# Optimization experiments

Measured on AMD Instinct MI355X. Metric: run time of the kernel, lower is better.

Reference implementation:

```python
import jax, jax.numpy as jnp
import numpy as np

EPS = 1e-6
HEADS = 8

def _ln_cf(x, w, b):
    # ConvNeXt-style channels_first LayerNorm over C axis of (B,C,H,W)
    mu = jnp.mean(x, axis=1, keepdims=True)
    var = jnp.mean((x - mu) ** 2, axis=1, keepdims=True)
    xn = (x - mu) / jnp.sqrt(var + EPS)
    return xn * w[None, :, None, None] + b[None, :, None, None]

def _xattn(q_map, kv_map, Wq, Wk, Wv, Wo, bo):
    B, C, H, W = q_map.shape
    HW = H * W
    dh = C // HEADS
    xq = q_map.reshape(B, C, HW).transpose(0, 2, 1)   # (B,HW,C)
    xkv = kv_map.reshape(B, C, HW).transpose(0, 2, 1)
    q = (xq @ Wq.T).reshape(B, HW, HEADS, dh).transpose(0, 2, 1, 3)
    k = (xkv @ Wk.T).reshape(B, HW, HEADS, dh).transpose(0, 2, 1, 3)
    v = (xkv @ Wv.T).reshape(B, HW, HEADS, dh).transpose(0, 2, 1, 3)
    scale = dh ** -0.5
    logits = jnp.einsum('bhqd,bhkd->bhqk', q, k) * scale
    attn = jax.nn.softmax(logits, axis=-1)
    o = jnp.einsum('bhqk,bhkd->bhqd', attn, v)        # (B,h,HW,dh)
    o = o.transpose(0, 2, 1, 3).reshape(B, HW, C)
    o = o @ Wo.T + bo
    return o.transpose(0, 2, 1).reshape(B, C, H, W)

def _ffn(x, W1, b1, W2, b2):
    # 1x1 convs == channel-wise linear; exact GELU (torch default)
    h = jnp.einsum('bchw,oc->bohw', x, W1) + b1[None, :, None, None]
    h = jax.nn.gelu(h, approximate=False)
    return jnp.einsum('bchw,oc->bohw', h, W2) + b2[None, :, None, None]

def setup_inputs() -> dict:
    key = jax.random.key(0)
    ks = jax.random.split(key, 24)
    B, C, H, W = 8, 512, 32, 32
    hid = 4 * C
    d = {
        'spatial_feat': jax.random.normal(ks[0], (B, C, H, W), jnp.float32),
        'freq_feat': jax.random.normal(ks[1], (B, C, H, W), jnp.float32),
        # spatial enhancer (standard cross-attn)
        's_Wq': jax.random.normal(ks[2], (C, C), jnp.float32) * 0.02,
        's_Wk': jax.random.normal(ks[3], (C, C), jnp.float32) * 0.02,
        's_Wv': jax.random.normal(ks[4], (C, C), jnp.float32) * 0.02,
        's_Wo': jax.random.normal(ks[5], (C, C), jnp.float32) * 0.02,
        's_bo': jnp.zeros((C,), jnp.float32),
        # frequency enhancer
        'f_Wq': jax.random.normal(ks[6], (C, C), jnp.float32) * 0.02,
        'f_Wk': jax.random.normal(ks[7], (C, C), jnp.float32) * 0.02,
        'f_Wv': jax.random.normal(ks[8], (C, C), jnp.float32) * 0.02,
        'f_Wo': jax.random.normal(ks[9], (C, C), jnp.float32) * 0.02,
        'f_bo': jnp.zeros((C,), jnp.float32),
        # norms
        'sn1_w': jnp.ones((C,), jnp.float32), 'sn1_b': jnp.zeros((C,), jnp.float32),
        'sn2_w': jnp.ones((C,), jnp.float32), 'sn2_b': jnp.zeros((C,), jnp.float32),
        'fn1_w': jnp.ones((C,), jnp.float32), 'fn1_b': jnp.zeros((C,), jnp.float32),
        'fn2_w': jnp.ones((C,), jnp.float32), 'fn2_b': jnp.zeros((C,), jnp.float32),
        # ConvFFNs (1x1 convs)
        'sffn_W1': jax.random.normal(ks[10], (hid, C), jnp.float32) * 0.02,
        'sffn_b1': jnp.zeros((hid,), jnp.float32),
        'sffn_W2': jax.random.normal(ks[11], (C, hid), jnp.float32) * 0.02,
        'sffn_b2': jnp.zeros((C,), jnp.float32),
        'fffn_W1': jax.random.normal(ks[12], (hid, C), jnp.float32) * 0.02,
        'fffn_b1': jnp.zeros((hid,), jnp.float32),
        'fffn_W2': jax.random.normal(ks[13], (C, hid), jnp.float32) * 0.02,
        'fffn_b2': jnp.zeros((C,), jnp.float32),
    }
    return d

def reference(spatial_feat, freq_feat,
              s_Wq, s_Wk, s_Wv, s_Wo, s_bo,
              f_Wq, f_Wk, f_Wv, f_Wo, f_bo,
              sn1_w, sn1_b, sn2_w, sn2_b,
              fn1_w, fn1_b, fn2_w, fn2_b,
              sffn_W1, sffn_b1, sffn_W2, sffn_b2,
              fffn_W1, fffn_b1, fffn_W2, fffn_b2):
    enh_s = _xattn(spatial_feat, freq_feat, s_Wq, s_Wk, s_Wv, s_Wo, s_bo)
    enh_f = _xattn(freq_feat, spatial_feat, f_Wq, f_Wk, f_Wv, f_Wo, f_bo)
    s = _ln_cf(spatial_feat + enh_s, sn1_w, sn1_b)
    s = _ln_cf(s + _ffn(s, sffn_W1, sffn_b1, sffn_W2, sffn_b2), sn2_w, sn2_b)
    f = _ln_cf(freq_feat + enh_f, fn1_w, fn1_b)
    f = _ln_cf(f + _ffn(f, fffn_W1, fffn_b1, fffn_W2, fffn_b2), fn2_w, fn2_b)
    return (s, f)
```

## Files before the change

kernel.cpp:

```cpp
#include <hip/hip_runtime.h>
#include <hip/hip_bf16.h>


#define CCH 512
#define HWD 1024

typedef unsigned short u16;
typedef unsigned int u32;
typedef __attribute__((ext_vector_type(8))) __bf16 bf16x8;
typedef __attribute__((ext_vector_type(4))) float f32x4;
typedef __attribute__((ext_vector_type(4))) unsigned short u16x4;
typedef __attribute__((ext_vector_type(8))) unsigned short u16x8;

__device__ __forceinline__ float bf2f(u16 u) { return __uint_as_float(((u32)u) << 16); }
__device__ __forceinline__ u16 f2bf(float f) {
    u32 u = __float_as_uint(f);
    return (u16)((u + 0x7fffu + ((u >> 16) & 1u)) >> 16);
}
__device__ __forceinline__ float ldp(const void* p, int i, bool isbf) {
    return isbf ? bf2f(((const u16*)p)[i]) : ((const float*)p)[i];
}
__device__ __forceinline__ float fast_gelu(float v) {
    return v * __frcp_rn(1.0f + __expf(-1.702f * v));
}

#define GLL16(g, l) __builtin_amdgcn_global_load_lds( \
    (const __attribute__((address_space(1))) u32*)(g), \
    (__attribute__((address_space(3))) u32*)(l), 16, 0, 0)

struct MMJob { const u16* A; const u16* W; const void* bias; void* Y; };
struct PJob  { const u16* A; const u16* W; u16* Y; int ldY; int gm; int gn; };
struct PJobs { PJob j[6]; };
struct AJob  { const u16* QK; const u16* VT; u16* AO; };
struct LNJob { const u16* A; const float* Br; const void* w; const void* b; void* Y; };

__global__ void k_detect(const u16* __restrict__ in, int* __restrict__ flag) {
    if (threadIdx.x == 0 && blockIdx.x == 0) {
        int sane = 0;
        for (int i = 0; i < 1024; i += 2) {
            int e = (in[i] >> 7) & 0xFF;
            if (e >= 0x6D && e <= 0x8D) sane++;
        }
        *flag = (sane >= 256) ? 1 : 0;
    }
}

struct CvtJobs {
    const void* src[12];
    u16* dst[12];
    int chunk0[13];
};
__global__ __launch_bounds__(256) void k_cvt_all(CvtJobs J, const int* __restrict__ flag) {
    bool isbf = (*flag != 0);
    int b = blockIdx.x;
    int j = 0;
    #pragma unroll
    for (int i = 0; i < 12; i++) if (b >= J.chunk0[i + 1]) j = i + 1;
    int idx = (b - J.chunk0[j]) * 1024 + threadIdx.x * 4;
    u16* d = J.dst[j] + idx;
    if (isbf) {
        *(u16x4*)d = *(const u16x4*)((const u16*)J.src[j] + idx);
    } else {
        float4 v = *(const float4*)((const float*)J.src[j] + idx);
        d[0] = f2bf(v.x); d[1] = f2bf(v.y); d[2] = f2bf(v.z); d[3] = f2bf(v.w);
    }
}

__global__ __launch_bounds__(256) void k_transpose2(const void* __restrict__ in0,
                                                    const void* __restrict__ in1,
                                                    u16* __restrict__ o0,
                                                    u16* __restrict__ o1,
                                                    const int* __restrict__ flag) {
    __shared__ float tile[32][33];
    bool isbf = (*flag != 0);
    int z = blockIdx.z;
    const void* in = (z < 8) ? in0 : in1;
    u16* out = (z < 8) ? o0 : o1;
    int b = z & 7;
    int hw0 = blockIdx.x * 32, c0 = blockIdx.y * 32;
    int tx = threadIdx.x, ty = threadIdx.y;
    size_t base = (size_t)b * CCH * HWD;
    if (isbf) {
        const u16* ip = (const u16*)in + base;
        for (int i = ty; i < 32; i += 8)
            tile[i][tx] = bf2f(ip[(size_t)(c0 + i) * HWD + hw0 + tx]);
    } else {
        const float* ip = (const float*)in + base;
        for (int i = ty; i < 32; i += 8)
            tile[i][tx] = ip[(size_t)(c0 + i) * HWD + hw0 + tx];
    }
    __syncthreads();
    u16* op = out + (size_t)b * HWD * CCH;
    for (int i = ty; i < 32; i += 8)
        op[(size_t)(hw0 + i) * CCH + c0 + tx] = f2bf(tile[tx][i]);
}

__device__ __forceinline__ void swz(int pid, int gm, int gn, int& bm, int& bn) {
    int gsz = 8 * gn;
    int gid = pid / gsz;
    int fm = gid * 8;
    int rows = (gm - fm < 8) ? (gm - fm) : 8;
    int pin = pid - gid * gsz;
    bm = fm + pin % rows;
    bn = pin / rows;
}

__global__ __launch_bounds__(256) void k_mm(MMJob j0, MMJob j1,
                                            int K, int ldY, int mode, int gm, int gn,
                                            const int* __restrict__ flag) {
    __shared__ u16 As[128 * 32], Asb[128 * 32];
    __shared__ u16 Bs[128 * 32], Bsb[128 * 32];
    MMJob J = blockIdx.z ? j1 : j0;
    int t = threadIdx.x;
    int w = t >> 6, l = t & 63;
    int bm, bn;
    swz(blockIdx.x, gm, gn, bm, bn);
    int m0 = bm * 128, n0 = bn * 128;
    int wm = (w >> 1) * 64, wn = (w & 1) * 64;

    int r0 = (w * 2 + 0) * 16 + (l >> 2);
    int r1 = (w * 2 + 1) * 16 + (l >> 2);
    int sg0 = (((l & 3) ^ ((r0 >> 1) & 3))) * 8;
    int sg1 = (((l & 3) ^ ((r1 >> 1) & 3))) * 8;
    const u16* ga0 = J.A + (size_t)(m0 + r0) * K + sg0;
    const u16* ga1 = J.A + (size_t)(m0 + r1) * K + sg1;
    const u16* gb0 = J.W + (size_t)(n0 + r0) * K + sg0;
    const u16* gb1 = J.W + (size_t)(n0 + r1) * K + sg1;
    int lo0 = (w * 2 + 0) * 512, lo1 = (w * 2 + 1) * 512;

    int quad = l >> 4, lr = l & 15;
    int aoff[4], boff[4];
    #pragma unroll
    for (int i = 0; i < 4; i++) {
        int ra = wm + i * 16 + lr, rb = wn + i * 16 + lr;
        aoff[i] = ra * 32 + (quad ^ ((ra >> 1) & 3)) * 8;
        boff[i] = rb * 32 + (quad ^ ((rb >> 1) & 3)) * 8;
    }

    f32x4 acc[4][4] = {};

    for (int k0 = 0; k0 < K; k0 += 64) {
        __syncthreads();
        GLL16(ga0 + k0, &As[lo0]);
        GLL16(ga1 + k0, &As[lo1]);
        GLL16(gb0 + k0, &Bs[lo0]);
        GLL16(gb1 + k0, &Bs[lo1]);
        GLL16(ga0 + k0 + 32, &Asb[lo0]);
        GLL16(ga1 + k0 + 32, &Asb[lo1]);
        GLL16(gb0 + k0 + 32, &Bsb[lo0]);
        GLL16(gb1 + k0 + 32, &Bsb[lo1]);
        __syncthreads();
        {
            bf16x8 af[4], bfr[4];
            #pragma unroll
            for (int i = 0; i < 4; i++) af[i] = *(const bf16x8*)&As[aoff[i]];
            #pragma unroll
            for (int j = 0; j < 4; j++) bfr[j] = *(const bf16x8*)&Bs[boff[j]];
            #pragma unroll
            for (int i = 0; i < 4; i++)
                #pragma unroll
                for (int j = 0; j < 4; j++)
                    acc[i][j] = __builtin_amdgcn_mfma_f32_16x16x32_bf16(af[i], bfr[j], acc[i][j], 0, 0, 0);
        }
        {
            bf16x8 af[4], bfr[4];
            #pragma unroll
            for (int i = 0; i < 4; i++) af[i] = *(const bf16x8*)&Asb[aoff[i]];
            #pragma unroll
            for (int j = 0; j < 4; j++) bfr[j] = *(const bf16x8*)&Bsb[boff[j]];
            #pragma unroll
            for (int i = 0; i < 4; i++)
                #pragma unroll
                for (int j = 0; j < 4; j++)
                    acc[i][j] = __builtin_amdgcn_mfma_f32_16x16x32_bf16(af[i], bfr[j], acc[i][j], 0, 0, 0);
        }
    }

    bool isbf = (*flag != 0);
    #pragma unroll
    for (int i = 0; i < 4; i++) {
        int rowb = m0 + wm + i * 16 + quad * 4;
        #pragma unroll
        for (int j = 0; j < 4; j++) {
            int col = n0 + wn + j * 16 + lr;
            float bv = (mode == 1 || mode == 2) ? ldp(J.bias, col, isbf) : 0.f;
            #pragma unroll
            for (int r = 0; r < 4; r++) {
                float v = acc[i][j][r] + bv;
                if (mode == 2) {
                    ((u16*)J.Y)[(size_t)(rowb + r) * ldY + col] = f2bf(fast_gelu(v));
                } else if (mode == 3) {
                    ((u16*)J.Y)[(size_t)(rowb + r) * ldY + col] = f2bf(v);
                } else {
                    ((float*)J.Y)[(size_t)(rowb + r) * ldY + col] = v;
                }
            }
        }
    }
}

__global__ __launch_bounds__(256) void k_mm64(MMJob j0, MMJob j1,
                                              int K, int ldY, int mode, int gm, int gn,
                                              const int* __restrict__ flag) {
    __shared__ u16 As[128 * 32], Asb[128 * 32];
    __shared__ u16 Bs[64 * 32], Bsb[64 * 32];
    MMJob J = blockIdx.z ? j1 : j0;
    int t = threadIdx.x;
    int w = t >> 6, l = t & 63;
    int bm, bn;
    swz(blockIdx.x, gm, gn, bm, bn);
    int m0 = bm * 128, n0 = bn * 64;
    int wm = (w >> 1) * 64, wn = (w & 1) * 32;

    int r0 = (w * 2 + 0) * 16 + (l >> 2);
    int r1 = (w * 2 + 1) * 16 + (l >> 2);
    int rb_ = w * 16 + (l >> 2);
    int sg0 = (((l & 3) ^ ((r0 >> 1) & 3))) * 8;
    int sg1 = (((l & 3) ^ ((r1 >> 1) & 3))) * 8;
    int sgb = (((l & 3) ^ ((rb_ >> 1) & 3))) * 8;
    const u16* ga0 = J.A + (size_t)(m0 + r0) * K + sg0;
    const u16* ga1 = J.A + (size_t)(m0 + r1) * K + sg1;
    const u16* gb  = J.W + (size_t)(n0 + rb_) * K + sgb;
    int lo0 = (w * 2 + 0) * 512, lo1 = (w * 2 + 1) * 512, lob = w * 512;

    int quad = l >> 4, lr = l & 15;
    int aoff[4], boff[2];
    #pragma unroll
    for (int i = 0; i < 4; i++) {
        int ra = wm + i * 16 + lr;
        aoff[i] = ra * 32 + (quad ^ ((ra >> 1) & 3)) * 8;
    }
    #pragma unroll
    for (int j = 0; j < 2; j++) {
        int rb2 = wn + j * 16 + lr;
        boff[j] = rb2 * 32 + (quad ^ ((rb2 >> 1) & 3)) * 8;
    }

    f32x4 acc[4][2] = {};

    for (int k0 = 0; k0 < K; k0 += 64) {
        __syncthreads();
        GLL16(ga0 + k0, &As[lo0]);
        GLL16(ga1 + k0, &As[lo1]);
        GLL16(gb + k0, &Bs[lob]);
        GLL16(ga0 + k0 + 32, &Asb[lo0]);
        GLL16(ga1 + k0 + 32, &Asb[lo1]);
        GLL16(gb + k0 + 32, &Bsb[lob]);
        __syncthreads();
        {
            bf16x8 af[4], bfr[2];
            #pragma unroll
            for (int i = 0; i < 4; i++) af[i] = *(const bf16x8*)&As[aoff[i]];
            #pragma unroll
            for (int j = 0; j < 2; j++) bfr[j] = *(const bf16x8*)&Bs[boff[j]];
            #pragma unroll
            for (int i = 0; i < 4; i++)
                #pragma unroll
                for (int j = 0; j < 2; j++)
                    acc[i][j] = __builtin_amdgcn_mfma_f32_16x16x32_bf16(af[i], bfr[j], acc[i][j], 0, 0, 0);
        }
        {
            bf16x8 af[4], bfr[2];
            #pragma unroll
            for (int i = 0; i < 4; i++) af[i] = *(const bf16x8*)&Asb[aoff[i]];
            #pragma unroll
            for (int j = 0; j < 2; j++) bfr[j] = *(const bf16x8*)&Bsb[boff[j]];
            #pragma unroll
            for (int i = 0; i < 4; i++)
                #pragma unroll
                for (int j = 0; j < 2; j++)
                    acc[i][j] = __builtin_amdgcn_mfma_f32_16x16x32_bf16(af[i], bfr[j], acc[i][j], 0, 0, 0);
        }
    }

    bool isbf = (*flag != 0);
    #pragma unroll
    for (int i = 0; i < 4; i++) {
        int rowb = m0 + wm + i * 16 + quad * 4;
        #pragma unroll
        for (int j = 0; j < 2; j++) {
            int col = n0 + wn + j * 16 + lr;
            float bv = (mode == 1 || mode == 2) ? ldp(J.bias, col, isbf) : 0.f;
            #pragma unroll
            for (int r = 0; r < 4; r++) {
                float v = acc[i][j][r] + bv;
                if (mode == 2) {
                    ((u16*)J.Y)[(size_t)(rowb + r) * ldY + col] = f2bf(fast_gelu(v));
                } else if (mode == 3) {
                    ((u16*)J.Y)[(size_t)(rowb + r) * ldY + col] = f2bf(v);
                } else {
                    ((float*)J.Y)[(size_t)(rowb + r) * ldY + col] = v;
                }
            }
        }
    }
}

__global__ __launch_bounds__(256) void k_proj(PJobs JJ, const int* __restrict__ flag) {
    __shared__ u16 As[128 * 32], Asb[128 * 32];
    __shared__ u16 Bs[64 * 32], Bsb[64 * 32];
    (void)flag;
    PJob J = JJ.j[blockIdx.z];
    const int K = 512;
    int t = threadIdx.x;
    int w = t >> 6, l = t & 63;
    int bm, bn;
    swz(blockIdx.x, J.gm, J.gn, bm, bn);
    int m0 = bm * 128, n0 = bn * 64;
    int wm = (w >> 1) * 64, wn = (w & 1) * 32;

    int r0 = (w * 2 + 0) * 16 + (l >> 2);
    int r1 = (w * 2 + 1) * 16 + (l >> 2);
    int rb_ = w * 16 + (l >> 2);
    int sg0 = (((l & 3) ^ ((r0 >> 1) & 3))) * 8;
    int sg1 = (((l & 3) ^ ((r1 >> 1) & 3))) * 8;
    int sgb = (((l & 3) ^ ((rb_ >> 1) & 3))) * 8;
    const u16* ga0 = J.A + (size_t)(m0 + r0) * K + sg0;
    const u16* ga1 = J.A + (size_t)(m0 + r1) * K + sg1;
    const u16* gb  = J.W + (size_t)(n0 + rb_) * K + sgb;
    int lo0 = (w * 2 + 0) * 512, lo1 = (w * 2 + 1) * 512, lob = w * 512;

    int quad = l >> 4, lr = l & 15;
    int aoff[4], boff[2];
    #pragma unroll
    for (int i = 0; i < 4; i++) {
        int ra = wm + i * 16 + lr;
        aoff[i] = ra * 32 + (quad ^ ((ra >> 1) & 3)) * 8;
    }
    #pragma unroll
    for (int j = 0; j < 2; j++) {
        int rb2 = wn + j * 16 + lr;
        boff[j] = rb2 * 32 + (quad ^ ((rb2 >> 1) & 3)) * 8;
    }

    f32x4 acc[4][2] = {};

    for (int k0 = 0; k0 < K; k0 += 64) {
        __syncthreads();
        GLL16(ga0 + k0, &As[lo0]);
        GLL16(ga1 + k0, &As[lo1]);
        GLL16(gb + k0, &Bs[lob]);
        GLL16(ga0 + k0 + 32, &Asb[lo0]);
        GLL16(ga1 + k0 + 32, &Asb[lo1]);
        GLL16(gb + k0 + 32, &Bsb[lob]);
        __syncthreads();
        {
            bf16x8 af[4], bfr[2];
            #pragma unroll
            for (int i = 0; i < 4; i++) af[i] = *(const bf16x8*)&As[aoff[i]];
            #pragma unroll
            for (int j = 0; j < 2; j++) bfr[j] = *(const bf16x8*)&Bs[boff[j]];
            #pragma unroll
            for (int i = 0; i < 4; i++)
                #pragma unroll
                for (int j = 0; j < 2; j++)
                    acc[i][j] = __builtin_amdgcn_mfma_f32_16x16x32_bf16(af[i], bfr[j], acc[i][j], 0, 0, 0);
        }
        {
            bf16x8 af[4], bfr[2];
            #pragma unroll
            for (int i = 0; i < 4; i++) af[i] = *(const bf16x8*)&Asb[aoff[i]];
            #pragma unroll
            for (int j = 0; j < 2; j++) bfr[j] = *(const bf16x8*)&Bsb[boff[j]];
            #pragma unroll
            for (int i = 0; i < 4; i++)
                #pragma unroll
                for (int j = 0; j < 2; j++)
                    acc[i][j] = __builtin_amdgcn_mfma_f32_16x16x32_bf16(af[i], bfr[j], acc[i][j], 0, 0, 0);
        }
    }

    #pragma unroll
    for (int i = 0; i < 4; i++) {
        int rowb = m0 + wm + i * 16 + quad * 4;
        #pragma unroll
        for (int j = 0; j < 2; j++) {
            int col = n0 + wn + j * 16 + lr;
            #pragma unroll
            for (int r = 0; r < 4; r++)
                J.Y[(size_t)(rowb + r) * J.ldY + col] = f2bf(acc[i][j][r]);
        }
    }
}

__global__ __launch_bounds__(256) void k_attn2(AJob j0, AJob j1) {
    __shared__ __align__(16) u16 Ks[2][64][32];
    __shared__ __align__(16) u16 Vs[2][64][32];
    __shared__ __align__(16) u16 U[10240];

    AJob J = blockIdx.y ? j1 : j0;
    int blk = blockIdx.x;
    int t = threadIdx.x;
    int w = t >> 6, l = t & 63;
    int l15 = l & 15, quad = l >> 4;
    int qt = blk >> 6;
    int bh = blk & 63;
    int h = bh & 7, b = bh >> 3;
    int tok0 = b * 1024;
    int q0 = qt * 128;
    int hc = h * 64;

    #pragma unroll
    for (int kc = 0; kc < 2; kc++)
        #pragma unroll
        for (int g = 0; g < 2; g++) {
            int row = w * 32 + g * 16 + (l >> 2);
            int sl = ((l & 3) ^ ((row >> 1) & 3)) * 8;
            const u16* gp = J.QK + (size_t)(tok0 + q0 + row) * 1024 + hc + kc * 32 + sl;
            GLL16(gp, &U[kc * 4096 + (w * 32 + g * 16) * 32]);
        }
    __syncthreads();

    bf16x8 qf[2][2];
    #pragma unroll
    for (int jq = 0; jq < 2; jq++)
        #pragma unroll
        for (int kc = 0; kc < 2; kc++) {
            int row = w * 32 + jq * 16 + l15;
            qf[jq][kc] = *(const bf16x8*)&U[kc * 4096 + row * 32 + (quad ^ ((row >> 1) & 3)) * 8];
        }

    u16* Pw = &U[w * 2560];

    float l_[2] = {0.f, 0.f};
    f32x4 acco[2][4] = {};

    for (int kt = 0; kt < 16; kt++) {
        __syncthreads();
        {
            int row = w * 16 + (l >> 2);
            int f = (row >> 1) & 3;
            int sl = ((l & 3) ^ f) * 8;
            int key = kt * 64 + row;
            #pragma unroll
            for (int kc = 0; kc < 2; kc++) {
                const u16* kp = J.QK + (size_t)(tok0 + key) * 1024 + 512 + hc + kc * 32 + sl;
                GLL16(kp, &Ks[kc][w * 16][0]);
            }
            #pragma unroll
            for (int kck = 0; kck < 2; kck++) {
                const u16* vp = J.VT + (size_t)(hc + row) * 8192 + tok0 + kt * 64 + kck * 32 + sl;
                GLL16(vp, &Vs[kck][w * 16][0]);
            }
        }
        __syncthreads();

        f32x4 accs[4][2] = {};
        #pragma unroll
        for (int kc = 0; kc < 2; kc++) {
            bf16x8 kf[4];
            #pragma unroll
            for (int i = 0; i < 4; i++) {
                int row = i * 16 + l15;
                kf[i] = *(const bf16x8*)&Ks[kc][row][(quad ^ ((row >> 1) & 3)) * 8];
            }
            #pragma unroll
            for (int i = 0; i < 4; i++)
                #pragma unroll
                for (int jq = 0; jq < 2; jq++)
                    accs[i][jq] = __builtin_amdgcn_mfma_f32_16x16x32_bf16(kf[i], qf[jq][kc], accs[i][jq], 0, 0, 0);
        }

        #pragma unroll
        for (int jq = 0; jq < 2; jq++) {
            float ts = 0.f;
            #pragma unroll
            for (int i = 0; i < 4; i++) {
                u16x4 pk;
                #pragma unroll
                for (int r = 0; r < 4; r++) {
                    float p = __expf(accs[i][jq][r] * 0.125f);
                    ts += p;
                    pk[r] = f2bf(p);
                }
                *(u16x4*)&Pw[(jq * 16 + l15) * 80 + i * 16 + quad * 4] = pk;
            }
            ts += __shfl_xor(ts, 16);
            ts += __shfl_xor(ts, 32);
            l_[jq] += ts;
        }

        #pragma unroll
        for (int kck = 0; kck < 2; kck++) {
            bf16x8 pf[2], vf[4];
            #pragma unroll
            for (int i2 = 0; i2 < 2; i2++)
                pf[i2] = *(const bf16x8*)&Pw[(i2 * 16 + l15) * 80 + kck * 32 + quad * 8];
            #pragma unroll
            for (int jd = 0; jd < 4; jd++) {
                int row = jd * 16 + l15;
                vf[jd] = *(const bf16x8*)&Vs[kck][row][(quad ^ ((row >> 1) & 3)) * 8];
            }
            #pragma unroll
            for (int i2 = 0; i2 < 2; i2++)
                #pragma unroll
                for (int jd = 0; jd < 4; jd++)
                    acco[i2][jd] = __builtin_amdgcn_mfma_f32_16x16x32_bf16(pf[i2], vf[jd], acco[i2][jd], 0, 0, 0);
        }
    }

    #pragma unroll
    for (int i2 = 0; i2 < 2; i2++) {
        float linv = 1.0f / l_[i2];
        #pragma unroll
        for (int r = 0; r < 4; r++) {
            float li = __shfl(linv, quad * 4 + r);
            int token = tok0 + q0 + w * 32 + i2 * 16 + quad * 4 + r;
            u16* dst = J.AO + (size_t)token * 512 + hc;
            #pragma unroll
            for (int jd = 0; jd < 4; jd++)
                dst[jd * 16 + l15] = f2bf(acco[i2][jd][r] * li);
        }
    }
}

__global__ __launch_bounds__(256) void k_ln(LNJob j0, LNJob j1,
                                            const int* __restrict__ flag) {
    LNJob J = blockIdx.y ? j1 : j0;
    bool isbf = (*flag != 0);
    int token = blockIdx.x * 4 + (threadIdx.x >> 6);
    int lane = threadIdx.x & 63;
    int c0 = lane * 8;
    const u16* pa = J.A + (size_t)token * CCH + c0;
    const float* pb = J.Br + (size_t)token * CCH + c0;
    u16x8 av = *(const u16x8*)pa;
    float4 b0 = *(const float4*)pb;
    float4 b1 = *(const float4*)(pb + 4);
    float v[8];
    float s = 0.f, s2 = 0.f;
    #pragma unroll
    for (int u = 0; u < 8; u++) {
        float x = bf2f(av[u]) + ((u < 4) ? (&b0.x)[u] : (&b1.x)[u - 4]);
        v[u] = x; s += x; s2 += x * x;
    }
    #pragma unroll
    for (int off = 32; off > 0; off >>= 1) {
        s += __shfl_xor(s, off);
        s2 += __shfl_xor(s2, off);
    }
    float mu = s * (1.f / CCH);
    float var = s2 * (1.f / CCH) - mu * mu;
    float rstd = rsqrtf(var + 1e-6f);
    u16x8 ov;
    #pragma unroll
    for (int u = 0; u < 8; u++)
        ov[u] = f2bf((v[u] - mu) * rstd * ldp(J.w, c0 + u, isbf) + ldp(J.b, c0 + u, isbf));
    *(u16x8*)((u16*)J.Y + (size_t)token * CCH + c0) = ov;
}

__global__ __launch_bounds__(256) void k_ln_out(LNJob j0, LNJob j1,
                                                void* __restrict__ out, int brBase,
                                                const int* __restrict__ flag) {
    LNJob J = blockIdx.y ? j1 : j0;
    int branch = brBase + blockIdx.y;
    bool isbf = (*flag != 0);
    int token = blockIdx.x * 4 + (threadIdx.x >> 6);
    int lane = threadIdx.x & 63;
    int c0 = lane * 8;
    const u16* pa = J.A + (size_t)token * CCH + c0;
    const float* pb = J.Br + (size_t)token * CCH + c0;
    u16x8 av = *(const u16x8*)pa;
    float4 b0 = *(const float4*)pb;
    float4 b1 = *(const float4*)(pb + 4);
    float v[8];
    float s = 0.f, s2 = 0.f;
    #pragma unroll
    for (int u = 0; u < 8; u++) {
        float x = bf2f(av[u]) + ((u < 4) ? (&b0.x)[u] : (&b1.x)[u - 4]);
        v[u] = x; s += x; s2 += x * x;
    }
    #pragma unroll
    for (int off = 32; off > 0; off >>= 1) {
        s += __shfl_xor(s, off);
        s2 += __shfl_xor(s2, off);
    }
    float mu = s * (1.f / CCH);
    float var = s2 * (1.f / CCH) - mu * mu;
    float rstd = rsqrtf(var + 1e-6f);
    int b = token >> 10, hw = token & 1023;
    size_t obase = (size_t)branch * CCH * HWD * 8 + (size_t)b * CCH * HWD + hw;
    if (isbf) {
        u16* op = (u16*)out + obase;
        #pragma unroll
        for (int u = 0; u < 8; u++) {
            float y = (v[u] - mu) * rstd * ldp(J.w, c0 + u, true) + ldp(J.b, c0 + u, true);
            op[(size_t)(c0 + u) * HWD] = f2bf(y);
        }
    } else {
        float* op = (float*)out + obase;
        #pragma unroll
        for (int u = 0; u < 8; u++) {
            float y = (v[u] - mu) * rstd * ldp(J.w, c0 + u, false) + ldp(J.b, c0 + u, false);
            op[(size_t)(c0 + u) * HWD] = y;
        }
    }
}

extern "C" void kernel_launch(void* const* d_in, const int* in_sizes, int n_in,
                              void* d_out, int out_size, void* d_ws, size_t ws_size,
                              hipStream_t stream) {
    (void)in_sizes; (void)n_in; (void)out_size;

    char* wsb = (char*)d_ws;
    int* flag = (int*)wsb;
    u16* Wall = (u16*)(wsb + 256);
    u16* Xs = (u16*)(wsb + 256 + 12582912);
    u16* Xf = (u16*)(wsb + 256 + 12582912 + 8388608);
    char* rbase = wsb + 29360384;

    const size_t BRSZ = 67108864;
    bool dual = ws_size >= (29360384 + 2 * BRSZ);

    u16* QKb[2]; u16* VTb[2]; u16* AOb[2]; u16* Hbb[2];
    float* ENHb[2];
    for (int b = 0; b < 2; b++) {
        char* r = rbase + (dual ? b * BRSZ : 0);
        QKb[b] = (u16*)r;
        ENHb[b] = (float*)r;
        VTb[b] = (u16*)(r + 16777216);
        AOb[b] = (u16*)(r + 16777216 + 8388608);
        Hbb[b] = (u16*)(r + 16777216 + 2 * 8388608);
    }

    const int SQ = 262144, SW1 = 1048576;
    const u16* Xq[2] = {Xs, Xf};
    const u16* Xkv[2] = {Xf, Xs};
    u16* Wq[2]; u16* Wk[2]; u16* Wv[2]; u16* Wo[2]; u16* W1[2]; u16* W2[2];
    const void *bo[2], *n1w[2], *n1b[2], *n2w[2], *n2b[2], *b1[2], *b2[2];
    for (int b = 0; b < 2; b++) {
        u16* Wb = Wall + (size_t)b * 3145728;
        Wq[b] = Wb; Wk[b] = Wb + SQ; Wv[b] = Wb + 2 * SQ; Wo[b] = Wb + 3 * SQ;
        W1[b] = Wb + 4 * SQ; W2[b] = Wb + 4 * SQ + SW1;
        bo[b]  = d_in[b ? 11 : 6];
        n1w[b] = d_in[b ? 16 : 12]; n1b[b] = d_in[b ? 17 : 13];
        n2w[b] = d_in[b ? 18 : 14]; n2b[b] = d_in[b ? 19 : 15];
        b1[b]  = d_in[b ? 25 : 21]; b2[b]  = d_in[b ? 27 : 23];
    }

    k_detect<<<1, 64, 0, stream>>>((const u16*)d_in[0], flag);

    {
        CvtJobs J;
        int ch = 0;
        for (int b = 0; b < 2; b++) {
            const int srcIdx[6] = {b ? 7 : 2, b ? 8 : 3, b ? 9 : 4, b ? 10 : 5,
                                   b ? 24 : 20, b ? 26 : 22};
            u16* dsts[6] = {Wq[b], Wk[b], Wv[b], Wo[b], W1[b], W2[b]};
            const int sz[6] = {SQ, SQ, SQ, SQ, SW1, SW1};
            for (int i = 0; i < 6; i++) {
                int j = b * 6 + i;
                J.src[j] = d_in[srcIdx[i]];
                J.dst[j] = dsts[i];
                J.chunk0[j] = ch;
                ch += sz[i] / 1024;
            }
        }
        J.chunk0[12] = ch;
        k_cvt_all<<<ch, 256, 0, stream>>>(J, flag);
    }

    dim3 tb(32, 8);
    k_transpose2<<<dim3(32, 16, 16), tb, 0, stream>>>(d_in[0], d_in[1], Xs, Xf, flag);

    auto mmj = [&](const u16* A, const u16* W, const void* bias, void* Y) {
        MMJob j; j.A = A; j.W = W; j.bias = bias; j.Y = Y; return j;
    };
    auto pj = [&](const u16* A, const u16* W, u16* Y, int ldY, int gm, int gn) {
        PJob j; j.A = A; j.W = W; j.Y = Y; j.ldY = ldY; j.gm = gm; j.gn = gn; return j;
    };
    auto lnj = [&](const u16* A, const float* Br, const void* w, const void* bb, void* Y) {
        LNJob j; j.A = A; j.Br = Br; j.w = w; j.b = bb; j.Y = Y; return j;
    };

    int nbr = dual ? 2 : 1;
    int nloop = dual ? 1 : 2;
    for (int it = 0; it < nloop; it++) {
        int b0 = dual ? 0 : it;
        int b1i = dual ? 1 : it;

        {
            PJobs JJ;
            int nz = 0;
            for (int z = 0; z < nbr; z++) {
                int b = dual ? z : it;
                JJ.j[nz++] = pj(Xq[b], Wq[b], QKb[b], 1024, 64, 8);
                JJ.j[nz++] = pj(Xkv[b], Wk[b], QKb[b] + 512, 1024, 64, 8);
                JJ.j[nz++] = pj(Wv[b], Xkv[b], VTb[b], 8192, 4, 128);
            }
            for (int z = nz; z < 6; z++) JJ.j[z] = JJ.j[0];
            k_proj<<<dim3(512, 1, nz), 256, 0, stream>>>(JJ, flag);
        }
        {
            AJob a0, a1;
            a0.QK = QKb[b0]; a0.VT = VTb[b0]; a0.AO = AOb[b0];
            a1.QK = QKb[b1i]; a1.VT = VTb[b1i]; a1.AO = AOb[b1i];
            k_attn2<<<dim3(512, nbr), 256, 0, stream>>>(a0, a1);
        }
        k_mm64<<<dim3(512, 1, nbr), 256, 0, stream>>>(
            mmj(AOb[b0], Wo[b0], bo[b0], ENHb[b0]),
            mmj(AOb[b1i], Wo[b1i], bo[b1i], ENHb[b1i]),
            512, 512, 1, 64, 8, flag);
        k_ln<<<dim3(2048, nbr), 256, 0, stream>>>(
            lnj(Xq[b0], ENHb[b0], n1w[b0], n1b[b0], AOb[b0]),
            lnj(Xq[b1i], ENHb[b1i], n1w[b1i], n1b[b1i], AOb[b1i]), flag);
        k_mm<<<dim3(1024, 1, nbr), 256, 0, stream>>>(
            mmj(AOb[b0], W1[b0], b1[b0], Hbb[b0]),
            mmj(AOb[b1i], W1[b1i], b1[b1i], Hbb[b1i]),
            512, 2048, 2, 64, 16, flag);
        k_mm64<<<dim3(512, 1, nbr), 256, 0, stream>>>(
            mmj(Hbb[b0], W2[b0], b2[b0], ENHb[b0]),
            mmj(Hbb[b1i], W2[b1i], b2[b1i], ENHb[b1i]),
            2048, 512, 1, 64, 8, flag);
        k_ln_out<<<dim3(2048, nbr), 256, 0, stream>>>(
            lnj(AOb[b0], ENHb[b0], n2w[b0], n2b[b0], nullptr),
            lnj(AOb[b1i], ENHb[b1i], n2w[b1i], n2b[b1i], nullptr),
            d_out, dual ? 0 : it, flag);
    }
}
```

Measured before the change: 508.5 us.

## Load GEMM B operand directly into registers and store residual branch in bf16

All three GEMM kernels (k_mm, k_mm64, k_proj) now load the weight (B) operand straight from global memory into registers instead of staging it through LDS with global_load_lds. This halves LDS use and removes LDS reads for B. The Wo and FFN2 GEMM outputs switch to bf16 (new mode 5) and the LayerNorm kernels read them as bf16, which halves that intermediate traffic. The costs are uncoalesced per-lane global loads of W and the extra rounding of the residual branch to bf16.

```diff
diff --git a/kernel.cpp b/kernel.cpp
--- a/kernel.cpp
+++ b/kernel.cpp
@@ -32,7 +32,7 @@
 struct PJob  { const u16* A; const u16* W; u16* Y; int ldY; int gm; int gn; };
 struct PJobs { PJob j[6]; };
 struct AJob  { const u16* QK; const u16* VT; u16* AO; };
-struct LNJob { const u16* A; const float* Br; const void* w; const void* b; void* Y; };
+struct LNJob { const u16* A; const u16* Br; const void* w; const void* b; void* Y; };
 
 __global__ void k_detect(const u16* __restrict__ in, int* __restrict__ flag) {
     if (threadIdx.x == 0 && blockIdx.x == 0) {
@@ -105,11 +105,20 @@
     bn = pin / rows;
 }
 
+__device__ __forceinline__ void ep_store(void* Y, size_t off, float v, int mode) {
+    if (mode == 2) {
+        ((u16*)Y)[off] = f2bf(fast_gelu(v));
+    } else if (mode == 3 || mode == 5) {
+        ((u16*)Y)[off] = f2bf(v);
+    } else {
+        ((float*)Y)[off] = v;
+    }
+}
+
 __global__ __launch_bounds__(256) void k_mm(MMJob j0, MMJob j1,
                                             int K, int ldY, int mode, int gm, int gn,
                                             const int* __restrict__ flag) {
     __shared__ u16 As[128 * 32], Asb[128 * 32];
-    __shared__ u16 Bs[128 * 32], Bsb[128 * 32];
     MMJob J = blockIdx.z ? j1 : j0;
     int t = threadIdx.x;
     int w = t >> 6, l = t & 63;
@@ -124,18 +133,19 @@
     int sg1 = (((l & 3) ^ ((r1 >> 1) & 3))) * 8;
     const u16* ga0 = J.A + (size_t)(m0 + r0) * K + sg0;
     const u16* ga1 = J.A + (size_t)(m0 + r1) * K + sg1;
-    const u16* gb0 = J.W + (size_t)(n0 + r0) * K + sg0;
-    const u16* gb1 = J.W + (size_t)(n0 + r1) * K + sg1;
     int lo0 = (w * 2 + 0) * 512, lo1 = (w * 2 + 1) * 512;
 
     int quad = l >> 4, lr = l & 15;
-    int aoff[4], boff[4];
+    int aoff[4];
     #pragma unroll
     for (int i = 0; i < 4; i++) {
-        int ra = wm + i * 16 + lr, rb = wn + i * 16 + lr;
+        int ra = wm + i * 16 + lr;
         aoff[i] = ra * 32 + (quad ^ ((ra >> 1) & 3)) * 8;
-        boff[i] = rb * 32 + (quad ^ ((rb >> 1) & 3)) * 8;
-    }
+    }
+    const u16* gwb[4];
+    #pragma unroll
+    for (int j = 0; j < 4; j++)
+        gwb[j] = J.W + (size_t)(n0 + wn + j * 16 + lr) * K + quad * 8;
 
     f32x4 acc[4][4] = {};
 
@@ -143,36 +153,34 @@
         __syncthreads();
         GLL16(ga0 + k0, &As[lo0]);
         GLL16(ga1 + k0, &As[lo1]);
-        GLL16(gb0 + k0, &Bs[lo0]);
-        GLL16(gb1 + k0, &Bs[lo1]);
         GLL16(ga0 + k0 + 32, &Asb[lo0]);
         GLL16(ga1 + k0 + 32, &Asb[lo1]);
-        GLL16(gb0 + k0 + 32, &Bsb[lo0]);
-        GLL16(gb1 + k0 + 32, &Bsb[lo1]);
-        __syncthreads();
-        {
-            bf16x8 af[4], bfr[4];
+        bf16x8 b0[4], b1[4];
+        #pragma unroll
+        for (int j = 0; j < 4; j++) {
+            b0[j] = *(const bf16x8*)(gwb[j] + k0);
+            b1[j] = *(const bf16x8*)(gwb[j] + k0 + 32);
+        }
+        __syncthreads();
+        {
+            bf16x8 af[4];
             #pragma unroll
             for (int i = 0; i < 4; i++) af[i] = *(const bf16x8*)&As[aoff[i]];
             #pragma unroll
-            for (int j = 0; j < 4; j++) bfr[j] = *(const bf16x8*)&Bs[boff[j]];
-            #pragma unroll
             for (int i = 0; i < 4; i++)
                 #pragma unroll
                 for (int j = 0; j < 4; j++)
-                    acc[i][j] = __builtin_amdgcn_mfma_f32_16x16x32_bf16(af[i], bfr[j], acc[i][j], 0, 0, 0);
-        }
-        {
-            bf16x8 af[4], bfr[4];
+                    acc[i][j] = __builtin_amdgcn_mfma_f32_16x16x32_bf16(af[i], b0[j], acc[i][j], 0, 0, 0);
+        }
+        {
+            bf16x8 af[4];
             #pragma unroll
             for (int i = 0; i < 4; i++) af[i] = *(const bf16x8*)&Asb[aoff[i]];
             #pragma unroll
-            for (int j = 0; j < 4; j++) bfr[j] = *(const bf16x8*)&Bsb[boff[j]];
-            #pragma unroll
             for (int i = 0; i < 4; i++)
                 #pragma unroll
                 for (int j = 0; j < 4; j++)
-                    acc[i][j] = __builtin_amdgcn_mfma_f32_16x16x32_bf16(af[i], bfr[j], acc[i][j], 0, 0, 0);
+                    acc[i][j] = __builtin_amdgcn_mfma_f32_16x16x32_bf16(af[i], b1[j], acc[i][j], 0, 0, 0);
         }
     }
 
@@ -183,18 +191,10 @@
         #pragma unroll
         for (int j = 0; j < 4; j++) {
             int col = n0 + wn + j * 16 + lr;
-            float bv = (mode == 1 || mode == 2) ? ldp(J.bias, col, isbf) : 0.f;
-            #pragma unroll
-            for (int r = 0; r < 4; r++) {
-                float v = acc[i][j][r] + bv;
-                if (mode == 2) {
-                    ((u16*)J.Y)[(size_t)(rowb + r) * ldY + col] = f2bf(fast_gelu(v));
-                } else if (mode == 3) {
-                    ((u16*)J.Y)[(size_t)(rowb + r) * ldY + col] = f2bf(v);
-                } else {
-                    ((float*)J.Y)[(size_t)(rowb + r) * ldY + col] = v;
-                }
-            }
+            float bv = (mode == 1 || mode == 2 || mode == 5) ? ldp(J.bias, col, isbf) : 0.f;
+            #pragma unroll
+            for (int r = 0; r < 4; r++)
+                ep_store(J.Y, (size_t)(rowb + r) * ldY + col, acc[i][j][r] + bv, mode);
         }
     }
 }
@@ -203,7 +203,6 @@
                                               int K, int ldY, int mode, int gm, int gn,
                                               const int* __restrict__ flag) {
     __shared__ u16 As[128 * 32], Asb[128 * 32];
-    __shared__ u16 Bs[64 * 32], Bsb[64 * 32];
     MMJob J = blockIdx.z ? j1 : j0;
     int t = threadIdx.x;
     int w = t >> 6, l = t & 63;
@@ -214,27 +213,23 @@
 
     int r0 = (w * 2 + 0) * 16 + (l >> 2);
     int r1 = (w * 2 + 1) * 16 + (l >> 2);
-    int rb_ = w * 16 + (l >> 2);
     int sg0 = (((l & 3) ^ ((r0 >> 1) & 3))) * 8;
     int sg1 = (((l & 3) ^ ((r1 >> 1) & 3))) * 8;
-    int sgb = (((l & 3) ^ ((rb_ >> 1) & 3))) * 8;
     const u16* ga0 = J.A + (size_t)(m0 + r0) * K + sg0;
     const u16* ga1 = J.A + (size_t)(m0 + r1) * K + sg1;
-    const u16* gb  = J.W + (size_t)(n0 + rb_) * K + sgb;
-    int lo0 = (w * 2 + 0) * 512, lo1 = (w * 2 + 1) * 512, lob = w * 512;
+    int lo0 = (w * 2 + 0) * 512, lo1 = (w * 2 + 1) * 512;
 
     int quad = l >> 4, lr = l & 15;
-    int aoff[4], boff[2];
+    int aoff[4];
     #pragma unroll
     for (int i = 0; i < 4; i++) {
         int ra = wm + i * 16 + lr;
         aoff[i] = ra * 32 + (quad ^ ((ra >> 1) & 3)) * 8;
     }
-    #pragma unroll
-    for (int j = 0; j < 2; j++) {
-        int rb2 = wn + j * 16 + lr;
-        boff[j] = rb2 * 32 + (quad ^ ((rb2 >> 1) & 3)) * 8;
-    }
+    const u16* gwb[2];
+    #pragma unroll
+    for (int j = 0; j < 2; j++)
+        gwb[j] = J.W + (size_t)(n0 + wn + j * 16 + lr) * K + quad * 8;
 
     f32x4 acc[4][2] = {};
 
@@ -242,34 +237,34 @@
         __syncthreads();
         GLL16(ga0 + k0, &As[lo0]);
         GLL16(ga1 + k0, &As[lo1]);
-        GLL16(gb + k0, &Bs[lob]);
         GLL16(ga0 + k0 + 32, &Asb[lo0]);
         GLL16(ga1 + k0 + 32, &Asb[lo1]);
-        GLL16(gb + k0 + 32, &Bsb[lob]);
-        __syncthreads();
-        {
-            bf16x8 af[4], bfr[2];
+        bf16x8 b0[2], b1[2];
+        #pragma unroll
+        for (int j = 0; j < 2; j++) {
+            b0[j] = *(const bf16x8*)(gwb[j] + k0);
+            b1[j] = *(const bf16x8*)(gwb[j] + k0 + 32);
+        }
+        __syncthreads();
+        {
+            bf16x8 af[4];
             #pragma unroll
             for (int i = 0; i < 4; i++) af[i] = *(const bf16x8*)&As[aoff[i]];
             #pragma unroll
-            for (int j = 0; j < 2; j++) bfr[j] = *(const bf16x8*)&Bs[boff[j]];
-            #pragma unroll
             for (int i = 0; i < 4; i++)
                 #pragma unroll
                 for (int j = 0; j < 2; j++)
-                    acc[i][j] = __builtin_amdgcn_mfma_f32_16x16x32_bf16(af[i], bfr[j], acc[i][j], 0, 0, 0);
-        }
-        {
-            bf16x8 af[4], bfr[2];
+                    acc[i][j] = __builtin_amdgcn_mfma_f32_16x16x32_bf16(af[i], b0[j], acc[i][j], 0, 0, 0);
+        }
+        {
+            bf16x8 af[4];
             #pragma unroll
             for (int i = 0; i < 4; i++) af[i] = *(const bf16x8*)&Asb[aoff[i]];
             #pragma unroll
-            for (int j = 0; j < 2; j++) bfr[j] = *(const bf16x8*)&Bsb[boff[j]];
-            #pragma unroll
             for (int i = 0; i < 4; i++)
                 #pragma unroll
                 for (int j = 0; j < 2; j++)
-                    acc[i][j] = __builtin_amdgcn_mfma_f32_16x16x32_bf16(af[i], bfr[j], acc[i][j], 0, 0, 0);
+                    acc[i][j] = __builtin_amdgcn_mfma_f32_16x16x32_bf16(af[i], b1[j], acc[i][j], 0, 0, 0);
         }
     }
 
@@ -280,25 +275,16 @@
         #pragma unroll
         for (int j = 0; j < 2; j++) {
             int col = n0 + wn + j * 16 + lr;
-            float bv = (mode == 1 || mode == 2) ? ldp(J.bias, col, isbf) : 0.f;
-            #pragma unroll
-            for (int r = 0; r < 4; r++) {
-                float v = acc[i][j][r] + bv;
-                if (mode == 2) {
-                    ((u16*)J.Y)[(size_t)(rowb + r) * ldY + col] = f2bf(fast_gelu(v));
-                } else if (mode == 3) {
-                    ((u16*)J.Y)[(size_t)(rowb + r) * ldY + col] = f2bf(v);
-                } else {
-                    ((float*)J.Y)[(size_t)(rowb + r) * ldY + col] = v;
-                }
-            }
+            float bv = (mode == 1 || mode == 2 || mode == 5) ? ldp(J.bias, col, isbf) : 0.f;
+            #pragma unroll
+            for (int r = 0; r < 4; r++)
+                ep_store(J.Y, (size_t)(rowb + r) * ldY + col, acc[i][j][r] + bv, mode);
         }
     }
 }
 
 __global__ __launch_bounds__(256) void k_proj(PJobs JJ, const int* __restrict__ flag) {
     __shared__ u16 As[128 * 32], Asb[128 * 32];
-    __shared__ u16 Bs[64 * 32], Bsb[64 * 32];
     (void)flag;
     PJob J = JJ.j[blockIdx.z];
     const int K = 512;
@@ -311,27 +297,23 @@
 
     int r0 = (w * 2 + 0) * 16 + (l >> 2);
     int r1 = (w * 2 + 1) * 16 + (l >> 2);
-    int rb_ = w * 16 + (l >> 2);
     int sg0 = (((l & 3) ^ ((r0 >> 1) & 3))) * 8;
     int sg1 = (((l & 3) ^ ((r1 >> 1) & 3))) * 8;
-    int sgb = (((l & 3) ^ ((rb_ >> 1) & 3))) * 8;
     const u16* ga0 = J.A + (size_t)(m0 + r0) * K + sg0;
     const u16* ga1 = J.A + (size_t)(m0 + r1) * K + sg1;
-    const u16* gb  = J.W + (size_t)(n0 + rb_) * K + sgb;
-    int lo0 = (w * 2 + 0) * 512, lo1 = (w * 2 + 1) * 512, lob = w * 512;
+    int lo0 = (w * 2 + 0) * 512, lo1 = (w * 2 + 1) * 512;
 
     int quad = l >> 4, lr = l & 15;
-    int aoff[4], boff[2];
+    int aoff[4];
     #pragma unroll
     for (int i = 0; i < 4; i++) {
         int ra = wm + i * 16 + lr;
         aoff[i] = ra * 32 + (quad ^ ((ra >> 1) & 3)) * 8;
     }
-    #pragma unroll
-    for (int j = 0; j < 2; j++) {
-        int rb2 = wn + j * 16 + lr;
-        boff[j] = rb2 * 32 + (quad ^ ((rb2 >> 1) & 3)) * 8;
-    }
+    const u16* gwb[2];
+    #pragma unroll
+    for (int j = 0; j < 2; j++)
+        gwb[j] = J.W + (size_t)(n0 + wn + j * 16 + lr) * K + quad * 8;
 
     f32x4 acc[4][2] = {};
 
@@ -339,34 +321,34 @@
         __syncthreads();
         GLL16(ga0 + k0, &As[lo0]);
         GLL16(ga1 + k0, &As[lo1]);
-        GLL16(gb + k0, &Bs[lob]);
         GLL16(ga0 + k0 + 32, &Asb[lo0]);
         GLL16(ga1 + k0 + 32, &Asb[lo1]);
-        GLL16(gb + k0 + 32, &Bsb[lob]);
-        __syncthreads();
-        {
-            bf16x8 af[4], bfr[2];
+        bf16x8 b0[2], b1[2];
+        #pragma unroll
+        for (int j = 0; j < 2; j++) {
+            b0[j] = *(const bf16x8*)(gwb[j] + k0);
+            b1[j] = *(const bf16x8*)(gwb[j] + k0 + 32);
+        }
+        __syncthreads();
+        {
+            bf16x8 af[4];
             #pragma unroll
             for (int i = 0; i < 4; i++) af[i] = *(const bf16x8*)&As[aoff[i]];
             #pragma unroll
-            for (int j = 0; j < 2; j++) bfr[j] = *(const bf16x8*)&Bs[boff[j]];
-            #pragma unroll
             for (int i = 0; i < 4; i++)
                 #pragma unroll
                 for (int j = 0; j < 2; j++)
-                    acc[i][j] = __builtin_amdgcn_mfma_f32_16x16x32_bf16(af[i], bfr[j], acc[i][j], 0, 0, 0);
-        }
-        {
-            bf16x8 af[4], bfr[2];
+                    acc[i][j] = __builtin_amdgcn_mfma_f32_16x16x32_bf16(af[i], b0[j], acc[i][j], 0, 0, 0);
+        }
+        {
+            bf16x8 af[4];
             #pragma unroll
             for (int i = 0; i < 4; i++) af[i] = *(const bf16x8*)&Asb[aoff[i]];
             #pragma unroll
-            for (int j = 0; j < 2; j++) bfr[j] = *(const bf16x8*)&Bsb[boff[j]];
-            #pragma unroll
             for (int i = 0; i < 4; i++)
                 #pragma unroll
                 for (int j = 0; j < 2; j++)
-                    acc[i][j] = __builtin_amdgcn_mfma_f32_16x16x32_bf16(af[i], bfr[j], acc[i][j], 0, 0, 0);
+                    acc[i][j] = __builtin_amdgcn_mfma_f32_16x16x32_bf16(af[i], b1[j], acc[i][j], 0, 0, 0);
         }
     }
 
@@ -521,16 +503,13 @@
     int token = blockIdx.x * 4 + (threadIdx.x >> 6);
     int lane = threadIdx.x & 63;
     int c0 = lane * 8;
-    const u16* pa = J.A + (size_t)token * CCH + c0;
-    const float* pb = J.Br + (size_t)token * CCH + c0;
-    u16x8 av = *(const u16x8*)pa;
-    float4 b0 = *(const float4*)pb;
-    float4 b1 = *(const float4*)(pb + 4);
+    u16x8 av = *(const u16x8*)(J.A + (size_t)token * CCH + c0);
+    u16x8 bv = *(const u16x8*)(J.Br + (size_t)token * CCH + c0);
     float v[8];
     float s = 0.f, s2 = 0.f;
     #pragma unroll
     for (int u = 0; u < 8; u++) {
-        float x = bf2f(av[u]) + ((u < 4) ? (&b0.x)[u] : (&b1.x)[u - 4]);
+        float x = bf2f(av[u]) + bf2f(bv[u]);
         v[u] = x; s += x; s2 += x * x;
     }
     #pragma unroll
@@ -557,16 +536,13 @@
     int token = blockIdx.x * 4 + (threadIdx.x >> 6);
     int lane = threadIdx.x & 63;
     int c0 = lane * 8;
-    const u16* pa = J.A + (size_t)token * CCH + c0;
-    const float* pb = J.Br + (size_t)token * CCH + c0;
-    u16x8 av = *(const u16x8*)pa;
-    float4 b0 = *(const float4*)pb;
-    float4 b1 = *(const float4*)(pb + 4);
+    u16x8 av = *(const u16x8*)(J.A + (size_t)token * CCH + c0);
+    u16x8 bvv = *(const u16x8*)(J.Br + (size_t)token * CCH + c0);
     float v[8];
     float s = 0.f, s2 = 0.f;
     #pragma unroll
     for (int u = 0; u < 8; u++) {
-        float x = bf2f(av[u]) + ((u < 4) ? (&b0.x)[u] : (&b1.x)[u - 4]);
+        float x = bf2f(av[u]) + bf2f(bvv[u]);
         v[u] = x; s += x; s2 += x * x;
     }
     #pragma unroll
@@ -611,12 +587,11 @@
     const size_t BRSZ = 67108864;
     bool dual = ws_size >= (29360384 + 2 * BRSZ);
 
-    u16* QKb[2]; u16* VTb[2]; u16* AOb[2]; u16* Hbb[2];
-    float* ENHb[2];
+    u16* QKb[2]; u16* VTb[2]; u16* AOb[2]; u16* Hbb[2]; u16* ENHb[2];
     for (int b = 0; b < 2; b++) {
         char* r = rbase + (dual ? b * BRSZ : 0);
         QKb[b] = (u16*)r;
-        ENHb[b] = (float*)r;
+        ENHb[b] = (u16*)r;
         VTb[b] = (u16*)(r + 16777216);
         AOb[b] = (u16*)(r + 16777216 + 8388608);
         Hbb[b] = (u16*)(r + 16777216 + 2 * 8388608);
@@ -668,7 +643,7 @@
     auto pj = [&](const u16* A, const u16* W, u16* Y, int ldY, int gm, int gn) {
         PJob j; j.A = A; j.W = W; j.Y = Y; j.ldY = ldY; j.gm = gm; j.gn = gn; return j;
     };
-    auto lnj = [&](const u16* A, const float* Br, const void* w, const void* bb, void* Y) {
+    auto lnj = [&](const u16* A, const u16* Br, const void* w, const void* bb, void* Y) {
         LNJob j; j.A = A; j.Br = Br; j.w = w; j.b = bb; j.Y = Y; return j;
     };
 
@@ -699,7 +674,7 @@
         k_mm64<<<dim3(512, 1, nbr), 256, 0, stream>>>(
             mmj(AOb[b0], Wo[b0], bo[b0], ENHb[b0]),
             mmj(AOb[b1i], Wo[b1i], bo[b1i], ENHb[b1i]),
-            512, 512, 1, 64, 8, flag);
+            512, 512, 5, 64, 8, flag);
         k_ln<<<dim3(2048, nbr), 256, 0, stream>>>(
             lnj(Xq[b0], ENHb[b0], n1w[b0], n1b[b0], AOb[b0]),
             lnj(Xq[b1i], ENHb[b1i], n1w[b1i], n1b[b1i], AOb[b1i]), flag);
@@ -710,7 +685,7 @@
         k_mm64<<<dim3(512, 1, nbr), 256, 0, stream>>>(
             mmj(Hbb[b0], W2[b0], b2[b0], ENHb[b0]),
             mmj(Hbb[b1i], W2[b1i], b2[b1i], ENHb[b1i]),
-            2048, 512, 1, 64, 8, flag);
+            2048, 512, 5, 64, 8, flag);
         k_ln_out<<<dim3(2048, nbr), 256, 0, stream>>>(
             lnj(AOb[b0], ENHb[b0], n2w[b0], n2b[b0], nullptr),
             lnj(AOb[b1i], ENHb[b1i], n2w[b1i], n2b[b1i], nullptr),
```

Measured after the change: 608.3 us. +19.6%, slower.
